# Optimization experiments

Measured on AMD Instinct MI355X. Metric: run time of the kernel, lower is better.

The kernel has to match this reference:

```python
import jax, jax.numpy as jnp
import numpy as np


def P1(X):
    # Projection onto {X : X @ 1 = 1, 1^T X = 1} under Frobenius norm.
    # Expanding the original matrix expression:
    #   P1(X)[i,j] = X[i,j] + 1/n + sum(X)/n^2 - row_sum[i]/n - col_sum[j]/n
    n = X.shape[1]
    row = X.sum(axis=1, keepdims=True)          # [n,1]
    col = X.sum(axis=0, keepdims=True)          # [1,n]
    s = row.sum()                               # scalar total
    return X + (1.0 / n + s / (n * n)) - row / n - col / n


def setup_inputs() -> dict:
    key = jax.random.key(0)
    n = 4096
    X = jax.random.normal(key, (n, n), dtype=jnp.float32)
    return {"X": X, "max_iters": 20}


def reference(X, max_iters):
    # Dykstra-style alternating projection: X <- P1(X); early-return if
    # min(X) >= 0, else X <- relu(X); up to max_iters iterations.
    # Fixed-length scan with a `done` flag reproduces the data-dependent
    # early exit while staying jit-compatible.
    def step(carry, _):
        Xc, done = carry
        Xp = P1(Xc)
        nonneg = jnp.min(Xp) >= 0
        # If converged this iter: return the un-relu'd projection; else relu.
        Xn = jnp.where(nonneg, Xp, jax.nn.relu(Xp))
        Xout = jnp.where(done, Xc, Xn)
        return (Xout, done | nonneg), None

    (Xf, _), _ = jax.lax.scan(step, (X, jnp.array(False)), None, length=max_iters)
    return Xf
```

## Files before the change

kernel.cpp:

```cpp
#include <hip/hip_runtime.h>


#define NN    4096
#define NV4   1024
#define NBLK  256
#define ITERS 20
#define INV_N (1.0f / 4096.0f)

typedef unsigned long long u64;
typedef float f32x4 __attribute__((ext_vector_type(4)));

__device__ __forceinline__ float wave_reduce_sum(float v) {
    #pragma unroll
    for (int m = 1; m < 64; m <<= 1) v += __shfl_xor(v, m, 64);
    return v;
}
__device__ __forceinline__ void st_b64(u64* p, u64 v) {
    __hip_atomic_store(p, v, __ATOMIC_RELAXED, __HIP_MEMORY_SCOPE_AGENT);
}
__device__ __forceinline__ u64 ld_b64(const u64* p) {
    return __hip_atomic_load(p, __ATOMIC_RELAXED, __HIP_MEMORY_SCOPE_AGENT);
}
__device__ __forceinline__ u64 packf2(float a, float b) {
    return (u64)__float_as_uint(a) | ((u64)__float_as_uint(b) << 32);
}
__device__ __forceinline__ float lo32(u64 u) { return __uint_as_float((unsigned)u); }
__device__ __forceinline__ float hi32(u64 u) { return __uint_as_float((unsigned)(u >> 32)); }

__global__ __launch_bounds__(1024, 4)
void persist9(const float* __restrict__ X0, float* __restrict__ Xout,
              u64* __restrict__ colF,
              u64* __restrict__ rowF,
              u64* __restrict__ pflag,
              u64* __restrict__ rdg)
{
    const int t    = threadIdx.x;
    const int lane = t & 63;
    const int g    = t >> 6;
    const int c    = lane;
    const int b    = blockIdx.x;
    const int bi   = b >> 4;
    const int bj   = b & 15;

    __shared__ float part[16][64][17];
    __shared__ f32x4 cq[16][64];
    __shared__ f32x4 rq4[16][64];
    __shared__ float bsv[256];
    __shared__ f32x4 colq[64];
    __shared__ float rsum[256];
    __shared__ float sG;

    f32x4 x[16];
    {
        const f32x4* xi = (const f32x4*)X0;
        const size_t base = (size_t)(bi * 256 + g * 16) * NV4 + (bj * 64 + c);
        #pragma unroll
        for (int r = 0; r < 16; ++r)
            x[r] = xi[base + (size_t)r * NV4];
    }

    for (int iter = 0; iter < ITERS; ++iter) {
        const int p = iter & 1;
        const u64 tagv = (u64)(iter + 1);

        if (iter >= 2) {
            if (lane < 16) {
                const u64 need = (u64)16 * (u64)(iter >> 1);
                const u64* f = rdg + (p * 16 + lane);
                while (ld_b64(f) < need) __builtin_amdgcn_s_sleep(1);
            }
            asm volatile("" ::: "memory");
        }

        f32x4 cacc = x[0];
        #pragma unroll
        for (int r = 1; r < 16; ++r) cacc += x[r];
        cq[g][c] = cacc;
        #pragma unroll
        for (int r = 0; r < 16; ++r)
            part[g][c][r] = (x[r].x + x[r].y) + (x[r].z + x[r].w);
        __syncthreads();

        float bs = 0.f;
        if (g == 0) {
            f32x4 v = cq[0][c];
            #pragma unroll
            for (int k = 1; k < 16; ++k) v += cq[k][c];
            u64* dst = colF + (((size_t)(p * NBLK + b)) << 7) + 2 * c;
            st_b64(dst,     packf2(v.x, v.y));
            st_b64(dst + 1, packf2(v.z, v.w));
            bs = wave_reduce_sum((v.x + v.y) + (v.z + v.w));
        }
        {
            const int r = lane & 15, q = lane >> 4;
            float v = 0.f;
            #pragma unroll
            for (int k = 0; k < 16; ++k) v += part[g][q * 16 + k][r];
            v += __shfl_xor(v, 16, 64);
            v += __shfl_xor(v, 32, 64);
            float vp = __shfl_xor(v, 1, 64);
            if (lane < 16 && (lane & 1) == 0) {
                u64* dst = rowF + (((size_t)(p * NBLK + b)) << 7) + 8 * g + (lane >> 1);
                st_b64(dst, packf2(v, vp));
            }
        }
        asm volatile("s_waitcnt vmcnt(0)" ::: "memory");
        __syncthreads();
        if (t == 0)
            st_b64(pflag + (p * NBLK + b),
                   (tagv << 32) | (u64)__float_as_uint(bs));

        const int fcsrc = g * 16 + bj;
        const int frsrc = bi * 16 + g;
        {
            const u64* fc = pflag + (p * NBLK + fcsrc);
            const u64* fr = pflag + (p * NBLK + frsrc);
            const u64* fb = pflag + (p * NBLK + (t & 255));
            bool dc = false, dr = false, db = (t >= 256);
            u64 ub = 0;
            while (true) {
                if (!dc && (ld_b64(fc) >> 32) == tagv) dc = true;
                if (!dr && (ld_b64(fr) >> 32) == tagv) dr = true;
                if (!db) { u64 u = ld_b64(fb);
                           if ((u >> 32) == tagv) { ub = u; db = true; } }
                if (dc && dr && db) break;
                __builtin_amdgcn_s_sleep(1);
            }
            if (t < 256) bsv[t] = lo32(ub);
        }
        asm volatile("" ::: "memory");
        {
            const u64* cp = colF + (((size_t)(p * NBLK + fcsrc)) << 7) + 2 * c;
            const u64* rp = rowF + (((size_t)(p * NBLK + frsrc)) << 7) + 2 * c;
            u64 c0 = ld_b64(cp), c1 = ld_b64(cp + 1);
            u64 r0 = ld_b64(rp), r1 = ld_b64(rp + 1);
            f32x4 cv, rv;
            cv.x = lo32(c0); cv.y = hi32(c0); cv.z = lo32(c1); cv.w = hi32(c1);
            rv.x = lo32(r0); rv.y = hi32(r0); rv.z = lo32(r1); rv.w = hi32(r1);
            cq[g][c]  = cv;
            rq4[g][c] = rv;
        }
        __syncthreads();
        if (t == 0)
            __hip_atomic_fetch_add(rdg + (p * 16 + bi), (u64)1,
                                   __ATOMIC_RELAXED, __HIP_MEMORY_SCOPE_AGENT);
        if (g == 0) {
            f32x4 v = cq[0][c];
            #pragma unroll
            for (int k = 1; k < 16; ++k) v += cq[k][c];
            colq[c] = v;
        } else if (g >= 4 && g < 8) {
            const int row = t - 256;
            const float* rqf = (const float*)rq4;
            float v = 0.f;
            #pragma unroll
            for (int k = 0; k < 16; ++k) v += rqf[k * 256 + row];
            rsum[row] = v;
        } else if (g == 8) {
            float v = bsv[lane] + bsv[64 + lane] + bsv[128 + lane] + bsv[192 + lane];
            v = wave_reduce_sum(v);
            if (lane == 0) sG = v;
        }
        __syncthreads();

        const float cc0 = INV_N + sG * (INV_N * INV_N);
        const f32x4 csub = colq[c] * INV_N;
        #pragma unroll
        for (int r = 0; r < 16; ++r) {
            const float a = cc0 - rsum[g * 16 + r] * INV_N;
            x[r].x = fmaxf(x[r].x + a - csub.x, 0.f);
            x[r].y = fmaxf(x[r].y + a - csub.y, 0.f);
            x[r].z = fmaxf(x[r].z + a - csub.z, 0.f);
            x[r].w = fmaxf(x[r].w + a - csub.w, 0.f);
        }
    }

    {
        f32x4* xo = (f32x4*)Xout;
        const size_t base = (size_t)(bi * 256 + g * 16) * NV4 + (bj * 64 + c);
        #pragma unroll
        for (int r = 0; r < 16; ++r)
            xo[base + (size_t)r * NV4] = x[r];
    }
}

extern "C" void kernel_launch(void* const* d_in, const int* in_sizes, int n_in,
                              void* d_out, int out_size, void* d_ws, size_t ws_size,
                              hipStream_t stream)
{
    const float* X0 = (const float*)d_in[0];
    float* X = (float*)d_out;

    u64* colF  = (u64*)d_ws;
    u64* rowF  = colF + 2 * NBLK * 128;
    u64* pflag = rowF + 2 * NBLK * 128;
    u64* rdg   = pflag + 2 * NBLK;

    hipMemsetAsync((void*)pflag, 0, (2 * NBLK + 2 * 16) * sizeof(u64), stream);

    persist9<<<dim3(NBLK), dim3(1024), 0, stream>>>(X0, X, colF, rowF,
                                                    pflag, rdg);
}
```

Measured before the change: 270.5 us.

## Replace reader-done counters with full flag barrier and pad per-block flags

```diff
diff --git a/kernel.cpp b/kernel.cpp
--- a/kernel.cpp
+++ b/kernel.cpp
@@ -28,11 +28,10 @@
 __device__ __forceinline__ float hi32(u64 u) { return __uint_as_float((unsigned)(u >> 32)); }
 
 __global__ __launch_bounds__(1024, 4)
-void persist9(const float* __restrict__ X0, float* __restrict__ Xout,
-              u64* __restrict__ colF,
-              u64* __restrict__ rowF,
-              u64* __restrict__ pflag,
-              u64* __restrict__ rdg)
+void persist10(const float* __restrict__ X0, float* __restrict__ Xout,
+               u64* __restrict__ colF,
+               u64* __restrict__ rowF,
+               u64* __restrict__ pflag)
 {
     const int t    = threadIdx.x;
     const int lane = t & 63;
@@ -62,15 +61,6 @@
     for (int iter = 0; iter < ITERS; ++iter) {
         const int p = iter & 1;
         const u64 tagv = (u64)(iter + 1);
-
-        if (iter >= 2) {
-            if (lane < 16) {
-                const u64 need = (u64)16 * (u64)(iter >> 1);
-                const u64* f = rdg + (p * 16 + lane);
-                while (ld_b64(f) < need) __builtin_amdgcn_s_sleep(1);
-            }
-            asm volatile("" ::: "memory");
-        }
 
         f32x4 cacc = x[0];
         #pragma unroll
@@ -107,28 +97,21 @@
         asm volatile("s_waitcnt vmcnt(0)" ::: "memory");
         __syncthreads();
         if (t == 0)
-            st_b64(pflag + (p * NBLK + b),
+            st_b64(pflag + ((size_t)(p * NBLK + b) << 3),
                    (tagv << 32) | (u64)__float_as_uint(bs));
+
+        if (t < 256) {
+            const u64* f = pflag + ((size_t)(p * NBLK + t) << 3);
+            u64 u;
+            while (((u = ld_b64(f)) >> 32) != tagv)
+                __builtin_amdgcn_s_sleep(1);
+            bsv[t] = lo32(u);
+        }
+        asm volatile("" ::: "memory");
+        __syncthreads();
 
         const int fcsrc = g * 16 + bj;
         const int frsrc = bi * 16 + g;
-        {
-            const u64* fc = pflag + (p * NBLK + fcsrc);
-            const u64* fr = pflag + (p * NBLK + frsrc);
-            const u64* fb = pflag + (p * NBLK + (t & 255));
-            bool dc = false, dr = false, db = (t >= 256);
-            u64 ub = 0;
-            while (true) {
-                if (!dc && (ld_b64(fc) >> 32) == tagv) dc = true;
-                if (!dr && (ld_b64(fr) >> 32) == tagv) dr = true;
-                if (!db) { u64 u = ld_b64(fb);
-                           if ((u >> 32) == tagv) { ub = u; db = true; } }
-                if (dc && dr && db) break;
-                __builtin_amdgcn_s_sleep(1);
-            }
-            if (t < 256) bsv[t] = lo32(ub);
-        }
-        asm volatile("" ::: "memory");
         {
             const u64* cp = colF + (((size_t)(p * NBLK + fcsrc)) << 7) + 2 * c;
             const u64* rp = rowF + (((size_t)(p * NBLK + frsrc)) << 7) + 2 * c;
@@ -141,9 +124,6 @@
             rq4[g][c] = rv;
         }
         __syncthreads();
-        if (t == 0)
-            __hip_atomic_fetch_add(rdg + (p * 16 + bi), (u64)1,
-                                   __ATOMIC_RELAXED, __HIP_MEMORY_SCOPE_AGENT);
         if (g == 0) {
             f32x4 v = cq[0][c];
             #pragma unroll
@@ -194,10 +174,8 @@
     u64* colF  = (u64*)d_ws;
     u64* rowF  = colF + 2 * NBLK * 128;
     u64* pflag = rowF + 2 * NBLK * 128;
-    u64* rdg   = pflag + 2 * NBLK;
 
-    hipMemsetAsync((void*)pflag, 0, (2 * NBLK + 2 * 16) * sizeof(u64), stream);
+    hipMemsetAsync((void*)pflag, 0, 2 * NBLK * 8 * sizeof(u64), stream);
 
-    persist9<<<dim3(NBLK), dim3(1024), 0, stream>>>(X0, X, colF, rowF,
-                                                    pflag, rdg);
+    persist10<<<dim3(NBLK), dim3(1024), 0, stream>>>(X0, X, colF, rowF, pflag);
 }
```

Result: faster. 250.1 us (-7.5%).
